# Performance work log

Hardware: AMD Instinct MI355X
Metric: run time of the kernel (lower is better)

The kernel has to match this reference:

```python
import jax, jax.numpy as jnp
import numpy as np

N_RAY, N_SAMPLES = 131072, 128
BIG_DELTA = 1e10
EPS = 1e-10


def setup_inputs() -> dict:
    key = jax.random.key(0)
    k1, k2, k3 = jax.random.split(key, 3)
    rgb = jax.random.uniform(k1, (N_RAY, N_SAMPLES, 3), dtype=jnp.float32)
    sigma = jax.random.normal(k2, (N_RAY, N_SAMPLES), dtype=jnp.float32)
    # sorted depths per ray in [2.0, 6.0), mimicking near/far bounds
    z_raw = jax.random.uniform(k3, (N_RAY, N_SAMPLES), dtype=jnp.float32, minval=2.0, maxval=6.0)
    z_vals = jnp.sort(z_raw, axis=-1)
    return {"rgb": rgb, "sigma": sigma, "z_vals": z_vals, "white_bkgd": 1}


def reference(rgb, sigma, z_vals, white_bkgd):
    # deltas: distance between adjacent samples, last one set to a huge value
    deltas = z_vals[:, 1:] - z_vals[:, :-1]
    deltas = jnp.concatenate(
        [deltas, jnp.full_like(deltas[:, :1], BIG_DELTA)], axis=-1)
    # sigma_activation = relu (opt.sigma_activation == 'relu')
    alpha = 1.0 - jnp.exp(-deltas * jax.nn.relu(sigma))
    # exclusive cumulative product of transmittance
    accum_prod = jnp.concatenate(
        [jnp.ones_like(alpha[:, :1]),
         jnp.cumprod(1.0 - alpha[:, :-1] + EPS, axis=-1)], axis=-1)
    weights = alpha * accum_prod                    # [N_ray, N_samples]
    comp_rgb = jnp.einsum('ns,nsc->nc', weights, rgb)  # [N_ray, 3]
    depth = jnp.sum(weights * z_vals, axis=-1)         # [N_ray]
    opacity = jnp.sum(weights, axis=-1)                # [N_ray]
    if white_bkgd:
        comp_rgb = comp_rgb + (1.0 - opacity[:, None])
    return comp_rgb, depth, opacity, weights
```

## Files before the change

### kernel.cpp

```cpp
#include <hip/hip_runtime.h>

#define N_RAY 131072
#define NS 128
#define BIG_DELTA 1e10f
#define EPS 1e-10f

__global__ __launch_bounds__(256) void volrender_kernel(
    const float* __restrict__ rgb,
    const float* __restrict__ sigma,
    const float* __restrict__ z_vals,
    const int* __restrict__ wb_flag,
    float* __restrict__ out)
{
    const int tid  = blockIdx.x * blockDim.x + threadIdx.x;
    const int ray  = tid >> 6;
    const int lane = tid & 63;
    if (ray >= N_RAY) return;

    const int base = ray * NS;

    float2 z  = *reinterpret_cast<const float2*>(&z_vals[base + 2 * lane]);
    float2 sg = *reinterpret_cast<const float2*>(&sigma [base + 2 * lane]);

    float z_next = __shfl_down(z.x, 1);
    float d0 = z.y - z.x;
    float d1 = (lane == 63) ? BIG_DELTA : (z_next - z.y);

    float a0 = 1.0f - expf(-d0 * fmaxf(sg.x, 0.0f));
    float a1 = 1.0f - expf(-d1 * fmaxf(sg.y, 0.0f));

    float t0 = 1.0f - a0 + EPS;
    float t1 = 1.0f - a1 + EPS;

    float p = t0 * t1;
    #pragma unroll
    for (int d = 1; d < 64; d <<= 1) {
        float q = __shfl_up(p, d);
        if (lane >= d) p *= q;
    }
    float e = __shfl_up(p, 1);
    if (lane == 0) e = 1.0f;

    float w0 = a0 * e;
    float w1 = a1 * (e * t0);

    float* wout = out + (size_t)N_RAY * 5 + base;
    *reinterpret_cast<float2*>(&wout[2 * lane]) = make_float2(w0, w1);

    const float* rp = rgb + (size_t)ray * (NS * 3) + 6 * lane;
    float2 c01 = *reinterpret_cast<const float2*>(rp);
    float2 c23 = *reinterpret_cast<const float2*>(rp + 2);
    float2 c45 = *reinterpret_cast<const float2*>(rp + 4);

    float r   = w0 * c01.x + w1 * c23.y;
    float g   = w0 * c01.y + w1 * c45.x;
    float b   = w0 * c23.x + w1 * c45.y;
    float dep = w0 * z.x   + w1 * z.y;
    float op  = w0 + w1;

    #pragma unroll
    for (int d = 32; d > 0; d >>= 1) {
        r   += __shfl_down(r, d);
        g   += __shfl_down(g, d);
        b   += __shfl_down(b, d);
        dep += __shfl_down(dep, d);
        op  += __shfl_down(op, d);
    }

    if (lane == 0) {
        const int wb = *wb_flag;
        const float add = wb ? (1.0f - op) : 0.0f;
        out[(size_t)ray * 3 + 0] = r + add;
        out[(size_t)ray * 3 + 1] = g + add;
        out[(size_t)ray * 3 + 2] = b + add;
        out[(size_t)N_RAY * 3 + ray] = dep;
        out[(size_t)N_RAY * 4 + ray] = op;
    }
}

extern "C" void kernel_launch(void* const* d_in, const int* in_sizes, int n_in,
                              void* d_out, int out_size, void* d_ws, size_t ws_size,
                              hipStream_t stream) {
    const float* rgb    = (const float*)d_in[0];
    const float* sigma  = (const float*)d_in[1];
    const float* z_vals = (const float*)d_in[2];
    const int*   wb     = (const int*)d_in[3];
    float* out = (float*)d_out;

    const int blocks = N_RAY / 4;
    volrender_kernel<<<blocks, 256, 0, stream>>>(rgb, sigma, z_vals, wb, out);
}
```

Measured before the change: 75.21 us.

## Process four samples per thread with 32 lanes per ray and float4 I/O

After: 79.40 us. 1.06x slower.

```diff
diff --git a/kernel.cpp b/kernel.cpp
--- a/kernel.cpp
+++ b/kernel.cpp
@@ -6,68 +6,76 @@
 #define EPS 1e-10f
 
 __global__ __launch_bounds__(256) void volrender_kernel(
-    const float* __restrict__ rgb,
-    const float* __restrict__ sigma,
-    const float* __restrict__ z_vals,
+    const float4* __restrict__ rgb4,
+    const float4* __restrict__ sigma4,
+    const float4* __restrict__ z4,
     const int* __restrict__ wb_flag,
     float* __restrict__ out)
 {
-    const int tid  = blockIdx.x * blockDim.x + threadIdx.x;
-    const int ray  = tid >> 6;
-    const int lane = tid & 63;
+    const int tid = blockIdx.x * blockDim.x + threadIdx.x;
+    const int ray = tid >> 5;
+    const int l   = threadIdx.x & 31;
     if (ray >= N_RAY) return;
 
-    const int base = ray * NS;
+    const float4 z = z4[(size_t)ray * 32 + l];
+    const float4 s = sigma4[(size_t)ray * 32 + l];
 
-    float2 z  = *reinterpret_cast<const float2*>(&z_vals[base + 2 * lane]);
-    float2 sg = *reinterpret_cast<const float2*>(&sigma [base + 2 * lane]);
+    float z_next = __shfl_down(z.x, 1, 32);
+    float d0 = z.y - z.x;
+    float d1 = z.z - z.y;
+    float d2 = z.w - z.z;
+    float d3 = (l == 31) ? BIG_DELTA : (z_next - z.w);
 
-    float z_next = __shfl_down(z.x, 1);
-    float d0 = z.y - z.x;
-    float d1 = (lane == 63) ? BIG_DELTA : (z_next - z.y);
-
-    float a0 = 1.0f - expf(-d0 * fmaxf(sg.x, 0.0f));
-    float a1 = 1.0f - expf(-d1 * fmaxf(sg.y, 0.0f));
+    float a0 = 1.0f - __expf(-d0 * fmaxf(s.x, 0.0f));
+    float a1 = 1.0f - __expf(-d1 * fmaxf(s.y, 0.0f));
+    float a2 = 1.0f - __expf(-d2 * fmaxf(s.z, 0.0f));
+    float a3 = 1.0f - __expf(-d3 * fmaxf(s.w, 0.0f));
 
     float t0 = 1.0f - a0 + EPS;
     float t1 = 1.0f - a1 + EPS;
+    float t2 = 1.0f - a2 + EPS;
+    float t3 = 1.0f - a3 + EPS;
 
-    float p = t0 * t1;
+    float p = (t0 * t1) * (t2 * t3);
     #pragma unroll
-    for (int d = 1; d < 64; d <<= 1) {
-        float q = __shfl_up(p, d);
-        if (lane >= d) p *= q;
+    for (int d = 1; d < 32; d <<= 1) {
+        float q = __shfl_up(p, d, 32);
+        if (l >= d) p *= q;
     }
-    float e = __shfl_up(p, 1);
-    if (lane == 0) e = 1.0f;
+    float e = __shfl_up(p, 1, 32);
+    if (l == 0) e = 1.0f;
 
     float w0 = a0 * e;
-    float w1 = a1 * (e * t0);
+    float e1 = e * t0;
+    float w1 = a1 * e1;
+    float e2 = e1 * t1;
+    float w2 = a2 * e2;
+    float w3 = a3 * (e2 * t2);
 
-    float* wout = out + (size_t)N_RAY * 5 + base;
-    *reinterpret_cast<float2*>(&wout[2 * lane]) = make_float2(w0, w1);
+    float4* wout = reinterpret_cast<float4*>(out + (size_t)N_RAY * 5) + (size_t)ray * 32 + l;
+    *wout = make_float4(w0, w1, w2, w3);
 
-    const float* rp = rgb + (size_t)ray * (NS * 3) + 6 * lane;
-    float2 c01 = *reinterpret_cast<const float2*>(rp);
-    float2 c23 = *reinterpret_cast<const float2*>(rp + 2);
-    float2 c45 = *reinterpret_cast<const float2*>(rp + 4);
+    const float4* rp = rgb4 + (size_t)ray * 96 + 3 * l;
+    float4 c0 = rp[0];
+    float4 c1 = rp[1];
+    float4 c2 = rp[2];
 
-    float r   = w0 * c01.x + w1 * c23.y;
-    float g   = w0 * c01.y + w1 * c45.x;
-    float b   = w0 * c23.x + w1 * c45.y;
-    float dep = w0 * z.x   + w1 * z.y;
-    float op  = w0 + w1;
+    float r   = w0 * c0.x + w1 * c0.w + w2 * c1.z + w3 * c2.y;
+    float g   = w0 * c0.y + w1 * c1.x + w2 * c1.w + w3 * c2.z;
+    float b   = w0 * c0.z + w1 * c1.y + w2 * c2.x + w3 * c2.w;
+    float dep = w0 * z.x  + w1 * z.y  + w2 * z.z  + w3 * z.w;
+    float op  = w0 + w1 + w2 + w3;
 
     #pragma unroll
-    for (int d = 32; d > 0; d >>= 1) {
-        r   += __shfl_down(r, d);
-        g   += __shfl_down(g, d);
-        b   += __shfl_down(b, d);
-        dep += __shfl_down(dep, d);
-        op  += __shfl_down(op, d);
+    for (int d = 16; d > 0; d >>= 1) {
+        r   += __shfl_down(r,   d, 32);
+        g   += __shfl_down(g,   d, 32);
+        b   += __shfl_down(b,   d, 32);
+        dep += __shfl_down(dep, d, 32);
+        op  += __shfl_down(op,  d, 32);
     }
 
-    if (lane == 0) {
+    if (l == 0) {
         const int wb = *wb_flag;
         const float add = wb ? (1.0f - op) : 0.0f;
         out[(size_t)ray * 3 + 0] = r + add;
@@ -81,12 +89,12 @@
 extern "C" void kernel_launch(void* const* d_in, const int* in_sizes, int n_in,
                               void* d_out, int out_size, void* d_ws, size_t ws_size,
                               hipStream_t stream) {
-    const float* rgb    = (const float*)d_in[0];
-    const float* sigma  = (const float*)d_in[1];
-    const float* z_vals = (const float*)d_in[2];
-    const int*   wb     = (const int*)d_in[3];
+    const float4* rgb    = (const float4*)d_in[0];
+    const float4* sigma  = (const float4*)d_in[1];
+    const float4* z_vals = (const float4*)d_in[2];
+    const int*    wb     = (const int*)d_in[3];
     float* out = (float*)d_out;
 
-    const int blocks = N_RAY / 4;
+    const int blocks = (N_RAY * 32) / 256;
     volrender_kernel<<<blocks, 256, 0, stream>>>(rgb, sigma, z_vals, wb, out);
 }
```

## Process four rays per wavefront with DPP scans and batched loads

Applied to the files above, without the earlier changes.

New measurement: 80.05 us, median of 3. 6.4% more time.

```diff
diff --git a/kernel.cpp b/kernel.cpp
--- a/kernel.cpp
+++ b/kernel.cpp
@@ -4,6 +4,30 @@
 #define NS 128
 #define BIG_DELTA 1e10f
 #define EPS 1e-10f
+
+#define DPPF(OLD, V, CTRL, RM) \
+  __int_as_float(__builtin_amdgcn_update_dpp(__float_as_int(OLD), __float_as_int(V), (CTRL), (RM), 0xf, false))
+
+
+__device__ __forceinline__ float mul_scan_incl(float p) {
+    p *= DPPF(1.0f, p, 0x111, 0xf);
+    p *= DPPF(1.0f, p, 0x112, 0xf);
+    p *= DPPF(1.0f, p, 0x114, 0xf);
+    p *= DPPF(1.0f, p, 0x118, 0xf);
+    p *= DPPF(1.0f, p, 0x142, 0xa);
+    p *= DPPF(1.0f, p, 0x143, 0xc);
+    return p;
+}
+
+__device__ __forceinline__ float wave_sum(float v) {
+    v += DPPF(0.0f, v, 0x111, 0xf);
+    v += DPPF(0.0f, v, 0x112, 0xf);
+    v += DPPF(0.0f, v, 0x114, 0xf);
+    v += DPPF(0.0f, v, 0x118, 0xf);
+    v += DPPF(0.0f, v, 0x142, 0xa);
+    v += DPPF(0.0f, v, 0x143, 0xc);
+    return __int_as_float(__builtin_amdgcn_readlane(__float_as_int(v), 63));
+}
 
 __global__ __launch_bounds__(256) void volrender_kernel(
     const float* __restrict__ rgb,
@@ -12,69 +36,76 @@
     const int* __restrict__ wb_flag,
     float* __restrict__ out)
 {
-    const int tid  = blockIdx.x * blockDim.x + threadIdx.x;
-    const int ray  = tid >> 6;
-    const int lane = tid & 63;
-    if (ray >= N_RAY) return;
+    const int lane = threadIdx.x & 63;
+    const int wid  = (blockIdx.x * blockDim.x + threadIdx.x) >> 6;
+    const size_t ray0 = (size_t)wid * 4;
 
-    const int base = ray * NS;
+    float2 zv[4], sv[4], c01[4], c23[4], c45[4];
+    #pragma unroll
+    for (int k = 0; k < 4; ++k) {
+        const size_t base = (ray0 + k) * NS + 2 * lane;
+        zv[k] = *reinterpret_cast<const float2*>(&z_vals[base]);
+        sv[k] = *reinterpret_cast<const float2*>(&sigma[base]);
+        const float* rp = rgb + (ray0 + k) * (NS * 3) + 6 * lane;
+        c01[k] = *reinterpret_cast<const float2*>(rp);
+        c23[k] = *reinterpret_cast<const float2*>(rp + 2);
+        c45[k] = *reinterpret_cast<const float2*>(rp + 4);
+    }
 
-    float2 z  = *reinterpret_cast<const float2*>(&z_vals[base + 2 * lane]);
-    float2 sg = *reinterpret_cast<const float2*>(&sigma [base + 2 * lane]);
-
-    float z_next = __shfl_down(z.x, 1);
-    float d0 = z.y - z.x;
-    float d1 = (lane == 63) ? BIG_DELTA : (z_next - z.y);
-
-    float a0 = 1.0f - expf(-d0 * fmaxf(sg.x, 0.0f));
-    float a1 = 1.0f - expf(-d1 * fmaxf(sg.y, 0.0f));
-
-    float t0 = 1.0f - a0 + EPS;
-    float t1 = 1.0f - a1 + EPS;
-
-    float p = t0 * t1;
-    #pragma unroll
-    for (int d = 1; d < 64; d <<= 1) {
-        float q = __shfl_up(p, d);
-        if (lane >= d) p *= q;
-    }
-    float e = __shfl_up(p, 1);
-    if (lane == 0) e = 1.0f;
-
-    float w0 = a0 * e;
-    float w1 = a1 * (e * t0);
-
-    float* wout = out + (size_t)N_RAY * 5 + base;
-    *reinterpret_cast<float2*>(&wout[2 * lane]) = make_float2(w0, w1);
-
-    const float* rp = rgb + (size_t)ray * (NS * 3) + 6 * lane;
-    float2 c01 = *reinterpret_cast<const float2*>(rp);
-    float2 c23 = *reinterpret_cast<const float2*>(rp + 2);
-    float2 c45 = *reinterpret_cast<const float2*>(rp + 4);
-
-    float r   = w0 * c01.x + w1 * c23.y;
-    float g   = w0 * c01.y + w1 * c45.x;
-    float b   = w0 * c23.x + w1 * c45.y;
-    float dep = w0 * z.x   + w1 * z.y;
-    float op  = w0 + w1;
+    float crs[4], cgs[4], cbs[4], dps[4], ops[4];
+    float* wout = out + (size_t)N_RAY * 5;
 
     #pragma unroll
-    for (int d = 32; d > 0; d >>= 1) {
-        r   += __shfl_down(r, d);
-        g   += __shfl_down(g, d);
-        b   += __shfl_down(b, d);
-        dep += __shfl_down(dep, d);
-        op  += __shfl_down(op, d);
+    for (int k = 0; k < 4; ++k) {
+        const float2 z = zv[k];
+        const float2 s = sv[k];
+
+        float znext = DPPF(0.0f, z.x, 0x130, 0xf);
+        float d0 = z.y - z.x;
+        float d1 = (lane == 63) ? BIG_DELTA : (znext - z.y);
+
+        float e0 = __expf(-d0 * fmaxf(s.x, 0.0f));
+        float e1 = __expf(-d1 * fmaxf(s.y, 0.0f));
+        float a0 = 1.0f - e0, a1 = 1.0f - e1;
+        float t0 = e0 + EPS,  t1 = e1 + EPS;
+
+        float p = mul_scan_incl(t0 * t1);
+        float E = DPPF(1.0f, p, 0x138, 0xf);
+
+        float w0 = a0 * E;
+        float w1 = a1 * (E * t0);
+
+        *reinterpret_cast<float2*>(&wout[(ray0 + k) * NS + 2 * lane]) =
+            make_float2(w0, w1);
+
+        float r   = w0 * c01[k].x + w1 * c23[k].y;
+        float g   = w0 * c01[k].y + w1 * c45[k].x;
+        float b   = w0 * c23[k].x + w1 * c45[k].y;
+        float dep = w0 * z.x      + w1 * z.y;
+        float op  = w0 + w1;
+
+        crs[k] = wave_sum(r);
+        cgs[k] = wave_sum(g);
+        cbs[k] = wave_sum(b);
+        dps[k] = wave_sum(dep);
+        ops[k] = wave_sum(op);
     }
 
     if (lane == 0) {
         const int wb = *wb_flag;
-        const float add = wb ? (1.0f - op) : 0.0f;
-        out[(size_t)ray * 3 + 0] = r + add;
-        out[(size_t)ray * 3 + 1] = g + add;
-        out[(size_t)ray * 3 + 2] = b + add;
-        out[(size_t)N_RAY * 3 + ray] = dep;
-        out[(size_t)N_RAY * 4 + ray] = op;
+        float ad[4];
+        #pragma unroll
+        for (int k = 0; k < 4; ++k) ad[k] = wb ? (1.0f - ops[k]) : 0.0f;
+
+        float4* co = reinterpret_cast<float4*>(out + (size_t)wid * 12);
+        co[0] = make_float4(crs[0] + ad[0], cgs[0] + ad[0], cbs[0] + ad[0], crs[1] + ad[1]);
+        co[1] = make_float4(cgs[1] + ad[1], cbs[1] + ad[1], crs[2] + ad[2], cgs[2] + ad[2]);
+        co[2] = make_float4(cbs[2] + ad[2], crs[3] + ad[3], cgs[3] + ad[3], cbs[3] + ad[3]);
+
+        reinterpret_cast<float4*>(out + (size_t)N_RAY * 3)[wid] =
+            make_float4(dps[0], dps[1], dps[2], dps[3]);
+        reinterpret_cast<float4*>(out + (size_t)N_RAY * 4)[wid] =
+            make_float4(ops[0], ops[1], ops[2], ops[3]);
     }
 }
 
@@ -87,6 +118,6 @@
     const int*   wb     = (const int*)d_in[3];
     float* out = (float*)d_out;
 
-    const int blocks = N_RAY / 4;
+    const int blocks = N_RAY / 16;
     volrender_kernel<<<blocks, 256, 0, stream>>>(rgb, sigma, z_vals, wb, out);
 }
```

## Use DPP wave scans, closed-form opacity, and hoist rgb loads

Applied to the files above, without the earlier changes.

Result: no change. 75.32 us (+0.2%).

```diff
diff --git a/kernel.cpp b/kernel.cpp
--- a/kernel.cpp
+++ b/kernel.cpp
@@ -4,6 +4,29 @@
 #define NS 128
 #define BIG_DELTA 1e10f
 #define EPS 1e-10f
+
+#define DPPF(OLD, V, CTRL, RM) \
+  __int_as_float(__builtin_amdgcn_update_dpp(__float_as_int(OLD), __float_as_int(V), (CTRL), (RM), 0xf, false))
+
+__device__ __forceinline__ float mul_scan_incl(float p) {
+    p *= DPPF(1.0f, p, 0x111, 0xf);
+    p *= DPPF(1.0f, p, 0x112, 0xf);
+    p *= DPPF(1.0f, p, 0x114, 0xf);
+    p *= DPPF(1.0f, p, 0x118, 0xf);
+    p *= DPPF(1.0f, p, 0x142, 0xa);
+    p *= DPPF(1.0f, p, 0x143, 0xc);
+    return p;
+}
+
+__device__ __forceinline__ float wave_sum63(float v) {
+    v += DPPF(0.0f, v, 0x111, 0xf);
+    v += DPPF(0.0f, v, 0x112, 0xf);
+    v += DPPF(0.0f, v, 0x114, 0xf);
+    v += DPPF(0.0f, v, 0x118, 0xf);
+    v += DPPF(0.0f, v, 0x142, 0xa);
+    v += DPPF(0.0f, v, 0x143, 0xc);
+    return v;
+}
 
 __global__ __launch_bounds__(256) void volrender_kernel(
     const float* __restrict__ rgb,
@@ -15,61 +38,47 @@
     const int tid  = blockIdx.x * blockDim.x + threadIdx.x;
     const int ray  = tid >> 6;
     const int lane = tid & 63;
-    if (ray >= N_RAY) return;
 
-    const int base = ray * NS;
+    const size_t base = (size_t)ray * NS + 2 * lane;
 
-    float2 z  = *reinterpret_cast<const float2*>(&z_vals[base + 2 * lane]);
-    float2 sg = *reinterpret_cast<const float2*>(&sigma [base + 2 * lane]);
+    const float2 z  = *reinterpret_cast<const float2*>(&z_vals[base]);
+    const float2 sg = *reinterpret_cast<const float2*>(&sigma[base]);
+    const float* rp = rgb + (size_t)ray * (NS * 3) + 6 * lane;
+    const float2 c01 = *reinterpret_cast<const float2*>(rp);
+    const float2 c23 = *reinterpret_cast<const float2*>(rp + 2);
+    const float2 c45 = *reinterpret_cast<const float2*>(rp + 4);
 
-    float z_next = __shfl_down(z.x, 1);
+    float znext = DPPF(0.0f, z.x, 0x130, 0xf);
     float d0 = z.y - z.x;
-    float d1 = (lane == 63) ? BIG_DELTA : (z_next - z.y);
+    float d1 = (lane == 63) ? BIG_DELTA : (znext - z.y);
 
-    float a0 = 1.0f - expf(-d0 * fmaxf(sg.x, 0.0f));
-    float a1 = 1.0f - expf(-d1 * fmaxf(sg.y, 0.0f));
+    float e0 = __expf(-d0 * fmaxf(sg.x, 0.0f));
+    float e1 = __expf(-d1 * fmaxf(sg.y, 0.0f));
+    float a0 = 1.0f - e0, a1 = 1.0f - e1;
+    float t0 = e0 + EPS,  t1 = e1 + EPS;
 
-    float t0 = 1.0f - a0 + EPS;
-    float t1 = 1.0f - a1 + EPS;
+    float p = mul_scan_incl(t0 * t1);
+    float E = DPPF(1.0f, p, 0x138, 0xf);
 
-    float p = t0 * t1;
-    #pragma unroll
-    for (int d = 1; d < 64; d <<= 1) {
-        float q = __shfl_up(p, d);
-        if (lane >= d) p *= q;
-    }
-    float e = __shfl_up(p, 1);
-    if (lane == 0) e = 1.0f;
+    float w0 = a0 * E;
+    float w1 = a1 * (E * t0);
 
-    float w0 = a0 * e;
-    float w1 = a1 * (e * t0);
-
-    float* wout = out + (size_t)N_RAY * 5 + base;
-    *reinterpret_cast<float2*>(&wout[2 * lane]) = make_float2(w0, w1);
-
-    const float* rp = rgb + (size_t)ray * (NS * 3) + 6 * lane;
-    float2 c01 = *reinterpret_cast<const float2*>(rp);
-    float2 c23 = *reinterpret_cast<const float2*>(rp + 2);
-    float2 c45 = *reinterpret_cast<const float2*>(rp + 4);
+    float* wout = out + (size_t)N_RAY * 5;
+    *reinterpret_cast<float2*>(&wout[base]) = make_float2(w0, w1);
 
     float r   = w0 * c01.x + w1 * c23.y;
     float g   = w0 * c01.y + w1 * c45.x;
     float b   = w0 * c23.x + w1 * c45.y;
     float dep = w0 * z.x   + w1 * z.y;
-    float op  = w0 + w1;
 
-    #pragma unroll
-    for (int d = 32; d > 0; d >>= 1) {
-        r   += __shfl_down(r, d);
-        g   += __shfl_down(g, d);
-        b   += __shfl_down(b, d);
-        dep += __shfl_down(dep, d);
-        op  += __shfl_down(op, d);
-    }
+    r   = wave_sum63(r);
+    g   = wave_sum63(g);
+    b   = wave_sum63(b);
+    dep = wave_sum63(dep);
 
-    if (lane == 0) {
-        const int wb = *wb_flag;
-        const float add = wb ? (1.0f - op) : 0.0f;
+    if (lane == 63) {
+        float op = 1.0f - p;
+        const float add = (*wb_flag) ? (1.0f - op) : 0.0f;
         out[(size_t)ray * 3 + 0] = r + add;
         out[(size_t)ray * 3 + 1] = g + add;
         out[(size_t)ray * 3 + 2] = b + add;
```
